# Kernel optimization log

Hardware: AMD Instinct MI355X
Metric: run time of the kernel (lower is better)

Reference implementation:

```python
import jax, jax.numpy as jnp
import numpy as np

HIDDEN = 2048
INTER = 5632
B, S = 2, 2048


def _ternary(key, shape):
    # values in {-1, 0, +1}, matching 2-bit packed ternary weights
    return jax.random.randint(key, shape, -1, 2).astype(jnp.float32)


def setup_inputs() -> dict:
    key = jax.random.key(0)
    ks = jax.random.split(key, 7)
    x = jax.random.normal(ks[0], (B, S, HIDDEN), dtype=jnp.float32)
    gate_w = _ternary(ks[1], (INTER, HIDDEN))   # [intermediate, hidden]
    up_w = _ternary(ks[2], (INTER, HIDDEN))     # [intermediate, hidden]
    down_w = _ternary(ks[3], (HIDDEN, INTER))   # [hidden, intermediate]
    # per-output-channel dequant scales (positive, as from absmean quantization)
    gate_s = jax.random.uniform(ks[4], (INTER,), minval=0.01, maxval=0.1, dtype=jnp.float32)
    up_s = jax.random.uniform(ks[5], (INTER,), minval=0.01, maxval=0.1, dtype=jnp.float32)
    down_s = jax.random.uniform(ks[6], (HIDDEN,), minval=0.01, maxval=0.1, dtype=jnp.float32)
    return {"x": x, "gate_w": gate_w, "up_w": up_w, "down_w": down_w,
            "gate_s": gate_s, "up_s": up_s, "down_s": down_s}


def reference(x, gate_w, up_w, down_w, gate_s, up_s, down_s):
    # x: (B, S, H) -> flatten tokens, as in forward_hidden
    b, s, h = x.shape
    xf = x.reshape(b * s, h)
    # ternary linear = add/sub-only matmul + per-channel scale
    g = jnp.einsum('th,ih->ti', xf, gate_w) * gate_s   # (T, I)
    u = jnp.einsum('th,ih->ti', xf, up_w) * up_s       # (T, I)
    hdn = jax.nn.silu(g) * u                            # gated activation
    out = jnp.einsum('ti,hi->th', hdn, down_w) * down_s  # (T, H)
    return out.reshape(b, s, -1)
```

## Files before the change

kernel.cpp:

```cpp
#include <hip/hip_runtime.h>
#include <stdint.h>
#include <stddef.h>

#define HIDDEN 2048
#define INTER  5632
#define TOKENS 4096
#define BKD    128
#define BKI    128
#define NT_GU  (HIDDEN / BKI)
#define NT_DN  (INTER / BKD)

typedef __attribute__((ext_vector_type(8))) _Float16 f16x8;
typedef __attribute__((ext_vector_type(4))) _Float16 f16x4;
typedef __attribute__((ext_vector_type(4))) float    f32x4;
typedef __attribute__((ext_vector_type(4))) int      i32x4;

__device__ __forceinline__ int swz8(int row, int q) {
    return row * 8 + ((q + row) & 7);
}

#define GLDS16(g, l) __builtin_amdgcn_global_load_lds( \
    (__attribute__((address_space(1))) void*)(g), \
    (__attribute__((address_space(3))) void*)(l), 16, 0, 0)

__device__ __forceinline__ int pack4i8(float4 f) {
    return ((int)(signed char)(int)f.x & 255)
         | (((int)(signed char)(int)f.y & 255) << 8)
         | (((int)(signed char)(int)f.z & 255) << 16)
         | (((int)(signed char)(int)f.w) << 24);
}

__global__ __launch_bounds__(256)
void prepass(const float* __restrict__ x,
             const float4* __restrict__ gw, const float4* __restrict__ uw,
             const float4* __restrict__ dw,
             int8_t* __restrict__ xq, float* __restrict__ xs,
             int* __restrict__ go, int* __restrict__ uo,
             _Float16* __restrict__ dno) {
    const int tid = threadIdx.x;
    if (blockIdx.x < 1024) {
        const int wave = tid >> 6;
        const int lane = tid & 63;
        const int t    = blockIdx.x * 4 + wave;
        const float4* row = (const float4*)(x + (size_t)t * HIDDEN);
        float4 v[8];
        #pragma unroll
        for (int j = 0; j < 8; ++j) v[j] = row[lane + 64 * j];
        float m = 0.0f;
        #pragma unroll
        for (int j = 0; j < 8; ++j) {
            m = fmaxf(m, fmaxf(fmaxf(fabsf(v[j].x), fabsf(v[j].y)),
                               fmaxf(fabsf(v[j].z), fabsf(v[j].w))));
        }
        #pragma unroll
        for (int off = 32; off; off >>= 1)
            m = fmaxf(m, __shfl_xor(m, off, 64));
        m = fmaxf(m, 1e-20f);
        if (lane == 0) xs[t] = m * (1.0f / 127.0f);
        const float inv = 127.0f / m;
        int* oq = (int*)(xq + (size_t)t * HIDDEN);
        #pragma unroll
        for (int j = 0; j < 8; ++j) {
            float4 f = v[j];
            f.x *= inv; f.y *= inv; f.z *= inv; f.w *= inv;
            float4 r;
            r.x = rintf(f.x); r.y = rintf(f.y); r.z = rintf(f.z); r.w = rintf(f.w);
            oq[lane + 64 * j] = pack4i8(r);
        }
        return;
    }
    const int NA = INTER * HIDDEN / 16;
    const int NC = INTER * HIDDEN / 8;
    const int stride = 2048 * 256;
    for (int u = (blockIdx.x - 1024) * 256 + tid; u < 2 * NA + NC; u += stride) {
        if (u < 2 * NA) {
            const bool is_g = u < NA;
            const int j = is_g ? u : u - NA;
            const float4* src = (is_g ? gw : uw) + (size_t)j * 4;
            float4 f0 = src[0], f1 = src[1], f2 = src[2], f3 = src[3];
            int4 p;
            p.x = pack4i8(f0); p.y = pack4i8(f1);
            p.z = pack4i8(f2); p.w = pack4i8(f3);
            ((int4*)(is_g ? go : uo))[j] = p;
        } else {
            const int j = u - 2 * NA;
            const float4* src = dw + (size_t)j * 2;
            float4 a = src[0], b = src[1];
            f16x8 o;
            o[0] = (_Float16)a.x; o[1] = (_Float16)a.y;
            o[2] = (_Float16)a.z; o[3] = (_Float16)a.w;
            o[4] = (_Float16)b.x; o[5] = (_Float16)b.y;
            o[6] = (_Float16)b.z; o[7] = (_Float16)b.w;
            *(f16x8*)(dno + (size_t)j * 8) = o;
        }
    }
}

__global__ __launch_bounds__(256, 2)
void gemm_gateup(const int8_t* __restrict__ Xq,
                 const int8_t* __restrict__ Wg,
                 const int8_t* __restrict__ Wu,
                 const float* __restrict__ xs,
                 const float* __restrict__ gs,
                 const float* __restrict__ us,
                 _Float16* __restrict__ Hm) {
    __shared__ int8_t As [128 * BKI];
    __shared__ int8_t Bgs[128 * BKI];
    __shared__ int8_t Bus[128 * BKI];

    const int pid   = (blockIdx.x % 8) * 176 + blockIdx.x / 8;
    const int local = pid % (16 * 44);
    const int bm    = ((pid / (16 * 44)) * 16 + (local & 15)) * 128;
    const int bn    = (local >> 4) * 128;

    const int tid  = threadIdx.x;
    const int lane = tid & 63;
    const int wave = tid >> 6;
    const int wm   = (wave >> 1) * 64;
    const int wn   = (wave & 1) * 64;
    const int l15  = lane & 15;
    const int lq   = lane >> 4;

    int rowA[4], sgA[4];
    #pragma unroll
    for (int j = 0; j < 4; ++j) {
        const int f = tid + 256 * j;
        rowA[j] = f >> 3;
        sgA[j]  = (((f & 7) - rowA[j]) & 7) * 16;
    }

    #define STG_GU(k0) do { \
        _Pragma("unroll") \
        for (int j = 0; j < 4; ++j) { \
            const int f_ = tid + 256 * j; \
            const int8_t* pX = Xq + (size_t)(bm + rowA[j]) * HIDDEN + (k0) + sgA[j]; \
            const int8_t* pG = Wg + (size_t)(bn + rowA[j]) * HIDDEN + (k0) + sgA[j]; \
            const int8_t* pU = Wu + (size_t)(bn + rowA[j]) * HIDDEN + (k0) + sgA[j]; \
            GLDS16(pX, &As [f_ * 16]); \
            GLDS16(pG, &Bgs[f_ * 16]); \
            GLDS16(pU, &Bus[f_ * 16]); \
        } \
    } while (0)

    i32x4 accg[4][4] = {};
    i32x4 accu[4][4] = {};

    STG_GU(0);
    __syncthreads();

    for (int t = 0; t < NT_GU; ++t) {
        i32x4 a[2][4], bg[2][4], bu[2][4];
        #pragma unroll
        for (int ks = 0; ks < 2; ++ks) {
            const int q = ks * 4 + lq;
            #pragma unroll
            for (int im = 0; im < 4; ++im)
                a[ks][im] = *(const i32x4*)&As[swz8(wm + im * 16 + l15, q) * 16];
            #pragma unroll
            for (int jn = 0; jn < 4; ++jn) {
                bg[ks][jn] = *(const i32x4*)&Bgs[swz8(wn + jn * 16 + l15, q) * 16];
                bu[ks][jn] = *(const i32x4*)&Bus[swz8(wn + jn * 16 + l15, q) * 16];
            }
        }
        __syncthreads();
        if (t + 1 < NT_GU) STG_GU((t + 1) * BKI);
        #pragma unroll
        for (int ks = 0; ks < 2; ++ks)
            #pragma unroll
            for (int jn = 0; jn < 4; ++jn)
                #pragma unroll
                for (int im = 0; im < 4; ++im) {
                    accg[im][jn] = __builtin_amdgcn_mfma_i32_16x16x64_i8(a[ks][im], bg[ks][jn], accg[im][jn], 0, 0, 0);
                    accu[im][jn] = __builtin_amdgcn_mfma_i32_16x16x64_i8(a[ks][im], bu[ks][jn], accu[im][jn], 0, 0, 0);
                }
        __syncthreads();
    }
    #undef STG_GU

    #pragma unroll
    for (int jn = 0; jn < 4; ++jn) {
        const int col = bn + wn + jn * 16 + l15;
        const float sg = gs[col];
        const float su = us[col];
        #pragma unroll
        for (int im = 0; im < 4; ++im) {
            const int rbase = bm + wm + im * 16 + lq * 4;
            #pragma unroll
            for (int r = 0; r < 4; ++r) {
                const int row = rbase + r;
                const float st = xs[row];
                float g = (float)accg[im][jn][r] * st * sg;
                float u = (float)accu[im][jn][r] * st * su;
                float h = (g / (1.0f + __expf(-g))) * u;
                Hm[(size_t)row * INTER + col] = (_Float16)h;
            }
        }
    }
}

__global__ __launch_bounds__(256, 2)
void gemm_down(const _Float16* __restrict__ Hm,
               const _Float16* __restrict__ Wd,
               const float* __restrict__ dsc,
               float* __restrict__ out) {
    __shared__ _Float16 As0[128 * 64];
    __shared__ _Float16 As1[128 * 64];
    __shared__ _Float16 Bs0[128 * 64];
    __shared__ _Float16 Bs1[128 * 64];

    const int pid = (blockIdx.x % 8) * 64 + blockIdx.x / 8;
    const int loc = pid & 255;
    const int bm  = ((pid >> 8) * 16 + (loc & 15)) * 128;
    const int bn  = (loc >> 4) * 128;

    const int tid  = threadIdx.x;
    const int lane = tid & 63;
    const int wave = tid >> 6;
    const int wm   = (wave >> 1) * 64;
    const int wn   = (wave & 1) * 64;
    const int l15  = lane & 15;
    const int lq   = lane >> 4;

    int rS[4], sS[4];
    #pragma unroll
    for (int j = 0; j < 4; ++j) {
        const int f = tid + 256 * j;
        rS[j] = f >> 3;
        sS[j] = (((f & 7) - (f >> 3)) & 7) * 8;
    }

    const _Float16* gA = Hm + (size_t)bm * INTER;
    const _Float16* gB = Wd + (size_t)bn * INTER;

    #define STG_DN(k0) do { \
        _Pragma("unroll") \
        for (int j = 0; j < 4; ++j) { \
            const int f_ = tid + 256 * j; \
            const size_t o_ = (size_t)rS[j] * INTER + (k0) + sS[j]; \
            GLDS16(gA + o_,      &As0[f_ * 8]); \
            GLDS16(gA + o_ + 64, &As1[f_ * 8]); \
            GLDS16(gB + o_,      &Bs0[f_ * 8]); \
            GLDS16(gB + o_ + 64, &Bs1[f_ * 8]); \
        } \
    } while (0)

    f32x4 acc[4][4] = {};

    STG_DN(0);
    __syncthreads();

    for (int t = 0; t < NT_DN; ++t) {
        f16x8 a[4][4], b[4][4];
        #pragma unroll
        for (int ks = 0; ks < 4; ++ks) {
            const _Float16* A_ = (ks < 2) ? As0 : As1;
            const _Float16* B_ = (ks < 2) ? Bs0 : Bs1;
            const int q = (ks & 1) * 4 + lq;
            #pragma unroll
            for (int im = 0; im < 4; ++im)
                a[ks][im] = *(const f16x8*)&A_[swz8(wm + im * 16 + l15, q) * 8];
            #pragma unroll
            for (int jn = 0; jn < 4; ++jn)
                b[ks][jn] = *(const f16x8*)&B_[swz8(wn + jn * 16 + l15, q) * 8];
        }
        __syncthreads();
        if (t + 1 < NT_DN) STG_DN((t + 1) * BKD);
        #pragma unroll
        for (int ks = 0; ks < 4; ++ks)
            #pragma unroll
            for (int jn = 0; jn < 4; ++jn)
                #pragma unroll
                for (int im = 0; im < 4; ++im)
                    acc[im][jn] = __builtin_amdgcn_mfma_f32_16x16x32_f16(a[ks][im], b[ks][jn], acc[im][jn], 0, 0, 0);
        __syncthreads();
    }
    #undef STG_DN

    #pragma unroll
    for (int jn = 0; jn < 4; ++jn) {
        const int col = bn + wn + jn * 16 + l15;
        const float sd = dsc[col];
        #pragma unroll
        for (int im = 0; im < 4; ++im) {
            const int rbase = bm + wm + im * 16 + lq * 4;
            #pragma unroll
            for (int r = 0; r < 4; ++r)
                out[(size_t)(rbase + r) * HIDDEN + col] = acc[im][jn][r] * sd;
        }
    }
}

extern "C" void kernel_launch(void* const* d_in, const int* in_sizes, int n_in,
                              void* d_out, int out_size, void* d_ws, size_t ws_size,
                              hipStream_t stream) {
    const float* x   = (const float*)d_in[0];
    const float* gw  = (const float*)d_in[1];
    const float* uw  = (const float*)d_in[2];
    const float* dw  = (const float*)d_in[3];
    const float* gsc = (const float*)d_in[4];
    const float* usc = (const float*)d_in[5];
    const float* dsc = (const float*)d_in[6];
    float* out = (float*)d_out;

    char* ws = (char*)d_ws;
    int8_t*   Xq  = (int8_t*)(ws);
    int8_t*   Wg8 = (int8_t*)(ws + 8388608ull);
    int8_t*   Wu8 = (int8_t*)(ws + 19922944ull);
    _Float16* Wdh = (_Float16*)(ws + 31457280ull);
    _Float16* Hm  = (_Float16*)(ws + 54525952ull);
    float*    xs  = (float*)(ws + 100663296ull);

    prepass<<<1024 + 2048, 256, 0, stream>>>(
        x, (const float4*)gw, (const float4*)uw, (const float4*)dw,
        Xq, xs, (int*)Wg8, (int*)Wu8, Wdh);

    gemm_gateup<<<(INTER / 128) * (TOKENS / 128), 256, 0, stream>>>(
        Xq, Wg8, Wu8, xs, gsc, usc, Hm);
    gemm_down<<<(HIDDEN / 128) * (TOKENS / 128), 256, 0, stream>>>(
        Hm, Wdh, dsc, out);
}
```

Baseline: 362.8 us.

## Double-buffer LDS and enlarge GEMM tiles to 256x128 with 512-thread blocks

Both GEMM kernels now use two LDS buffers, so the next K-tile's global-to-LDS loads are issued before the MFMAs on the current tile, which drops one barrier per iteration. Block tiles grow to 256 rows by 128 columns with 8 waves, raising per-block reuse of the weight tile, and the down GEMM's K step shrinks to 64. The block-index swizzle is simplified to match the new grid. The cost is much more LDS per block (about 128KB for gate/up), which likely limits occupancy to one block per CU and ties the loads to a single barrier per step.

```diff
diff --git a/kernel.cpp b/kernel.cpp
--- a/kernel.cpp
+++ b/kernel.cpp
@@ -5,15 +5,15 @@
 #define HIDDEN 2048
 #define INTER  5632
 #define TOKENS 4096
-#define BKD    128
+#define BKD    64
 #define BKI    128
 #define NT_GU  (HIDDEN / BKI)
 #define NT_DN  (INTER / BKD)
 
-typedef __attribute__((ext_vector_type(8))) _Float16 f16x8;
-typedef __attribute__((ext_vector_type(4))) _Float16 f16x4;
-typedef __attribute__((ext_vector_type(4))) float    f32x4;
-typedef __attribute__((ext_vector_type(4))) int      i32x4;
+typedef __attribute__((ext_vector_type(8)))  _Float16 f16x8;
+typedef __attribute__((ext_vector_type(4)))  _Float16 f16x4;
+typedef __attribute__((ext_vector_type(4)))  float    f32x4;
+typedef __attribute__((ext_vector_type(4)))  int      i32x4;
 
 __device__ __forceinline__ int swz8(int row, int q) {
     return row * 8 + ((q + row) & 7);
@@ -96,7 +96,7 @@
     }
 }
 
-__global__ __launch_bounds__(256, 2)
+__global__ __launch_bounds__(512, 2)
 void gemm_gateup(const int8_t* __restrict__ Xq,
                  const int8_t* __restrict__ Wg,
                  const int8_t* __restrict__ Wu,
@@ -104,14 +104,13 @@
                  const float* __restrict__ gs,
                  const float* __restrict__ us,
                  _Float16* __restrict__ Hm) {
-    __shared__ int8_t As [128 * BKI];
-    __shared__ int8_t Bgs[128 * BKI];
-    __shared__ int8_t Bus[128 * BKI];
-
-    const int pid   = (blockIdx.x % 8) * 176 + blockIdx.x / 8;
-    const int local = pid % (16 * 44);
-    const int bm    = ((pid / (16 * 44)) * 16 + (local & 15)) * 128;
-    const int bn    = (local >> 4) * 128;
+    __shared__ int8_t As [2][256 * BKI];
+    __shared__ int8_t Bgs[2][128 * BKI];
+    __shared__ int8_t Bus[2][128 * BKI];
+
+    const int pid = (blockIdx.x % 8) * 88 + blockIdx.x / 8;
+    const int bm  = (pid & 15) * 256;
+    const int bn  = (pid >> 4) * 128;
 
     const int tid  = threadIdx.x;
     const int lane = tid & 63;
@@ -121,49 +120,56 @@
     const int l15  = lane & 15;
     const int lq   = lane >> 4;
 
-    int rowA[4], sgA[4];
+    int rowS[4], segS[4];
     #pragma unroll
     for (int j = 0; j < 4; ++j) {
-        const int f = tid + 256 * j;
-        rowA[j] = f >> 3;
-        sgA[j]  = (((f & 7) - rowA[j]) & 7) * 16;
-    }
-
-    #define STG_GU(k0) do { \
+        const int f = tid + 512 * j;
+        rowS[j] = f >> 3;
+        segS[j] = (((f & 7) - (f >> 3)) & 7) * 16;
+    }
+
+    #define STG_GU(b, k0) do { \
         _Pragma("unroll") \
         for (int j = 0; j < 4; ++j) { \
-            const int f_ = tid + 256 * j; \
-            const int8_t* pX = Xq + (size_t)(bm + rowA[j]) * HIDDEN + (k0) + sgA[j]; \
-            const int8_t* pG = Wg + (size_t)(bn + rowA[j]) * HIDDEN + (k0) + sgA[j]; \
-            const int8_t* pU = Wu + (size_t)(bn + rowA[j]) * HIDDEN + (k0) + sgA[j]; \
-            GLDS16(pX, &As [f_ * 16]); \
-            GLDS16(pG, &Bgs[f_ * 16]); \
-            GLDS16(pU, &Bus[f_ * 16]); \
+            const int f_ = tid + 512 * j; \
+            GLDS16(Xq + (size_t)(bm + rowS[j]) * HIDDEN + (k0) + segS[j], \
+                   &As[b][f_ * 16]); \
+        } \
+        _Pragma("unroll") \
+        for (int j = 0; j < 2; ++j) { \
+            const int f_ = tid + 512 * j; \
+            const size_t o_ = (size_t)(bn + rowS[j]) * HIDDEN + (k0) + segS[j]; \
+            GLDS16(Wg + o_, &Bgs[b][f_ * 16]); \
+            GLDS16(Wu + o_, &Bus[b][f_ * 16]); \
         } \
     } while (0)
 
     i32x4 accg[4][4] = {};
     i32x4 accu[4][4] = {};
 
-    STG_GU(0);
+    STG_GU(0, 0);
     __syncthreads();
 
+    int cur = 0;
     for (int t = 0; t < NT_GU; ++t) {
+        const int8_t* A_ = As [cur];
+        const int8_t* G_ = Bgs[cur];
+        const int8_t* U_ = Bus[cur];
+
         i32x4 a[2][4], bg[2][4], bu[2][4];
         #pragma unroll
         for (int ks = 0; ks < 2; ++ks) {
             const int q = ks * 4 + lq;
             #pragma unroll
             for (int im = 0; im < 4; ++im)
-                a[ks][im] = *(const i32x4*)&As[swz8(wm + im * 16 + l15, q) * 16];
+                a[ks][im] = *(const i32x4*)&A_[swz8(wm + im * 16 + l15, q) * 16];
             #pragma unroll
             for (int jn = 0; jn < 4; ++jn) {
-                bg[ks][jn] = *(const i32x4*)&Bgs[swz8(wn + jn * 16 + l15, q) * 16];
-                bu[ks][jn] = *(const i32x4*)&Bus[swz8(wn + jn * 16 + l15, q) * 16];
+                bg[ks][jn] = *(const i32x4*)&G_[swz8(wn + jn * 16 + l15, q) * 16];
+                bu[ks][jn] = *(const i32x4*)&U_[swz8(wn + jn * 16 + l15, q) * 16];
             }
         }
-        __syncthreads();
-        if (t + 1 < NT_GU) STG_GU((t + 1) * BKI);
+        if (t + 1 < NT_GU) STG_GU(cur ^ 1, (t + 1) * BKI);
         #pragma unroll
         for (int ks = 0; ks < 2; ++ks)
             #pragma unroll
@@ -174,6 +180,7 @@
                     accu[im][jn] = __builtin_amdgcn_mfma_i32_16x16x64_i8(a[ks][im], bu[ks][jn], accu[im][jn], 0, 0, 0);
                 }
         __syncthreads();
+        cur ^= 1;
     }
     #undef STG_GU
 
@@ -198,20 +205,17 @@
     }
 }
 
-__global__ __launch_bounds__(256, 2)
+__global__ __launch_bounds__(512, 2)
 void gemm_down(const _Float16* __restrict__ Hm,
                const _Float16* __restrict__ Wd,
                const float* __restrict__ dsc,
                float* __restrict__ out) {
-    __shared__ _Float16 As0[128 * 64];
-    __shared__ _Float16 As1[128 * 64];
-    __shared__ _Float16 Bs0[128 * 64];
-    __shared__ _Float16 Bs1[128 * 64];
-
-    const int pid = (blockIdx.x % 8) * 64 + blockIdx.x / 8;
-    const int loc = pid & 255;
-    const int bm  = ((pid >> 8) * 16 + (loc & 15)) * 128;
-    const int bn  = (loc >> 4) * 128;
+    __shared__ _Float16 As[2][256 * BKD];
+    __shared__ _Float16 Bs[2][128 * BKD];
+
+    const int pid = (blockIdx.x % 8) * 32 + blockIdx.x / 8;
+    const int bm  = (pid & 15) * 256;
+    const int bn  = (pid >> 4) * 128;
 
     const int tid  = threadIdx.x;
     const int lane = tid & 63;
@@ -221,41 +225,43 @@
     const int l15  = lane & 15;
     const int lq   = lane >> 4;
 
-    int rS[4], sS[4];
+    int rowS[4], segS[4];
     #pragma unroll
     for (int j = 0; j < 4; ++j) {
-        const int f = tid + 256 * j;
-        rS[j] = f >> 3;
-        sS[j] = (((f & 7) - (f >> 3)) & 7) * 8;
-    }
-
-    const _Float16* gA = Hm + (size_t)bm * INTER;
-    const _Float16* gB = Wd + (size_t)bn * INTER;
-
-    #define STG_DN(k0) do { \
+        const int f = tid + 512 * j;
+        rowS[j] = f >> 3;
+        segS[j] = (((f & 7) - (f >> 3)) & 7) * 8;
+    }
+
+    #define STG_DN(b, k0) do { \
         _Pragma("unroll") \
         for (int j = 0; j < 4; ++j) { \
-            const int f_ = tid + 256 * j; \
-            const size_t o_ = (size_t)rS[j] * INTER + (k0) + sS[j]; \
-            GLDS16(gA + o_,      &As0[f_ * 8]); \
-            GLDS16(gA + o_ + 64, &As1[f_ * 8]); \
-            GLDS16(gB + o_,      &Bs0[f_ * 8]); \
-            GLDS16(gB + o_ + 64, &Bs1[f_ * 8]); \
+            const int f_ = tid + 512 * j; \
+            GLDS16(Hm + (size_t)(bm + rowS[j]) * INTER + (k0) + segS[j], \
+                   &As[b][f_ * 8]); \
+        } \
+        _Pragma("unroll") \
+        for (int j = 0; j < 2; ++j) { \
+            const int f_ = tid + 512 * j; \
+            GLDS16(Wd + (size_t)(bn + rowS[j]) * INTER + (k0) + segS[j], \
+                   &Bs[b][f_ * 8]); \
         } \
     } while (0)
 
     f32x4 acc[4][4] = {};
 
-    STG_DN(0);
+    STG_DN(0, 0);
     __syncthreads();
 
+    int cur = 0;
     for (int t = 0; t < NT_DN; ++t) {
-        f16x8 a[4][4], b[4][4];
-        #pragma unroll
-        for (int ks = 0; ks < 4; ++ks) {
-            const _Float16* A_ = (ks < 2) ? As0 : As1;
-            const _Float16* B_ = (ks < 2) ? Bs0 : Bs1;
-            const int q = (ks & 1) * 4 + lq;
+        const _Float16* A_ = As[cur];
+        const _Float16* B_ = Bs[cur];
+
+        f16x8 a[2][4], b[2][4];
+        #pragma unroll
+        for (int ks = 0; ks < 2; ++ks) {
+            const int q = ks * 4 + lq;
             #pragma unroll
             for (int im = 0; im < 4; ++im)
                 a[ks][im] = *(const f16x8*)&A_[swz8(wm + im * 16 + l15, q) * 8];
@@ -263,16 +269,16 @@
             for (int jn = 0; jn < 4; ++jn)
                 b[ks][jn] = *(const f16x8*)&B_[swz8(wn + jn * 16 + l15, q) * 8];
         }
-        __syncthreads();
-        if (t + 1 < NT_DN) STG_DN((t + 1) * BKD);
-        #pragma unroll
-        for (int ks = 0; ks < 4; ++ks)
+        if (t + 1 < NT_DN) STG_DN(cur ^ 1, (t + 1) * BKD);
+        #pragma unroll
+        for (int ks = 0; ks < 2; ++ks)
             #pragma unroll
             for (int jn = 0; jn < 4; ++jn)
                 #pragma unroll
                 for (int im = 0; im < 4; ++im)
                     acc[im][jn] = __builtin_amdgcn_mfma_f32_16x16x32_f16(a[ks][im], b[ks][jn], acc[im][jn], 0, 0, 0);
         __syncthreads();
+        cur ^= 1;
     }
     #undef STG_DN
 
@@ -314,8 +320,8 @@
         x, (const float4*)gw, (const float4*)uw, (const float4*)dw,
         Xq, xs, (int*)Wg8, (int*)Wu8, Wdh);
 
-    gemm_gateup<<<(INTER / 128) * (TOKENS / 128), 256, 0, stream>>>(
+    gemm_gateup<<<(INTER / 128) * (TOKENS / 256), 512, 0, stream>>>(
         Xq, Wg8, Wu8, xs, gsc, usc, Hm);
-    gemm_down<<<(HIDDEN / 128) * (TOKENS / 128), 256, 0, stream>>>(
+    gemm_down<<<(HIDDEN / 128) * (TOKENS / 256), 512, 0, stream>>>(
         Hm, Wdh, dsc, out);
 }
```

After: 403.3 us. +11.2%, slower.
